# Kernel tuning notes

Measured on AMD Instinct MI355X. Metric: run time of the kernel, lower is better.

Reference implementation:

```python
import jax, jax.numpy as jnp
import numpy as np

N = 50000        # drug nodes
R = 64           # relations (side effects)
E = 20000        # edges per relation
B = 16           # bases
IN = 256
OUT = 256


def setup_inputs() -> dict:
    key = jax.random.key(0)
    ks = jax.random.split(key, 7)
    x = jax.random.normal(ks[0], (N, IN), dtype=jnp.float32)
    att = jax.random.normal(ks[1], (R, B), dtype=jnp.float32) / np.sqrt(B)
    basis = jax.random.normal(ks[2], (B, IN, OUT), dtype=jnp.float32) / np.sqrt(IN)
    root = jax.random.normal(ks[3], (IN, OUT), dtype=jnp.float32) / np.sqrt(IN)
    # per-destination-node degree normalizer (strictly positive, like edge counts)
    dest_deg = jax.random.uniform(ks[4], (N, 1), dtype=jnp.float32) * 9.0 + 1.0
    edge_src = jax.random.randint(ks[5], (R, E), 0, N, dtype=jnp.int64)
    edge_dst = jax.random.randint(ks[6], (R, E), 0, N, dtype=jnp.int64)
    return {"x": x, "att": att, "basis": basis, "root": root,
            "dest_deg": dest_deg, "edge_src": edge_src, "edge_dst": edge_dst}


def reference(x, att, basis, root, dest_deg, edge_src, edge_dst):
    # basis decomposition: w[r] = sum_b att[r,b] * basis[b]
    w = jnp.einsum('rb,bio->rio', att, basis)          # [R, IN, OUT]
    # per-relation gather + transform: messages along each edge
    x_src = x[edge_src]                                 # [R, E, IN]
    msgs = jnp.einsum('rei,rio->reo', x_src, w)         # [R, E, OUT]
    # scatter-sum to destinations, summed over all relations (HeteroConv aggr='sum')
    agg = jax.ops.segment_sum(msgs.reshape(-1, OUT),
                              edge_dst.reshape(-1),
                              num_segments=N)           # [N, OUT]
    out = agg / dest_deg + x @ root                     # [N, OUT]
    return out
```

## Files before the change

### kernel.cpp

```cpp
#include <hip/hip_runtime.h>
#include <stdint.h>

#define NN 50000
#define RR 64
#define EE 20000
#define NB 16
#define IND 256
#define OUTD 256
#define KK 4352
#define NE (RR * EE)
#define GITER 68
#define SCANB 49

typedef __attribute__((ext_vector_type(8))) short bf16x8;
typedef __attribute__((ext_vector_type(4))) float f32x4;
typedef __attribute__((ext_vector_type(2))) float f32x2;
typedef __attribute__((ext_vector_type(2))) unsigned int u32x2;

__device__ __forceinline__ unsigned short f2bf(float f) {
  union { float f; unsigned u; } v; v.f = f;
  unsigned r = v.u + 0x7FFFu + ((v.u >> 16) & 1u);
  return (unsigned short)(r >> 16);
}
__device__ __forceinline__ float asf(unsigned u) {
  union { unsigned u; float f; } v; v.u = u; return v.f;
}

__global__ __launch_bounds__(256) void k_xbf(const float* __restrict__ x,
                                             unsigned short* __restrict__ xsw) {
  const int gt = blockIdx.x * 256 + threadIdx.x;
  const size_t g = (size_t)gt * 8;
  const int row = gt >> 5;
  const int k = (gt & 31) * 8;
  float4 v0 = *reinterpret_cast<const float4*>(x + g);
  float4 v1 = *reinterpret_cast<const float4*>(x + g + 4);
  union { bf16x8 v; unsigned short u[8]; } pk;
  pk.u[0]=f2bf(v0.x); pk.u[1]=f2bf(v0.y); pk.u[2]=f2bf(v0.z); pk.u[3]=f2bf(v0.w);
  pk.u[4]=f2bf(v1.x); pk.u[5]=f2bf(v1.y); pk.u[6]=f2bf(v1.z); pk.u[7]=f2bf(v1.w);
  const int tile = k >> 6, ch = (k >> 3) & 7;
  *reinterpret_cast<bf16x8*>(
      xsw + (size_t)row * 256 + tile * 64 + ((ch ^ (row & 7)) << 3)) = pk.v;
}

__global__ __launch_bounds__(256) void k_hist(const int* __restrict__ edst,
                                              int* __restrict__ cnt) {
  const int g = blockIdx.x * 256 + threadIdx.x;
  atomicAdd(&cnt[edst[g]], 1);
}

__global__ __launch_bounds__(256) void k_scan_a(const int* __restrict__ cnt,
                                                int* __restrict__ rowptr,
                                                int* __restrict__ bsum) {
  __shared__ int ps[256];
  const int t = threadIdx.x, blk = blockIdx.x;
  const int base = blk * 1024 + t * 4;
  int v[4];
#pragma unroll
  for (int q = 0; q < 4; ++q) {
    const int idx = base + q;
    v[q] = (idx < NN) ? cnt[idx] : 0;
  }
  const int s = v[0] + v[1] + v[2] + v[3];
  ps[t] = s;
  __syncthreads();
  for (int off = 1; off < 256; off <<= 1) {
    const int u = (t >= off) ? ps[t - off] : 0;
    __syncthreads();
    ps[t] += u;
    __syncthreads();
  }
  int run = ps[t] - s;
#pragma unroll
  for (int q = 0; q < 4; ++q) {
    const int idx = base + q;
    if (idx < NN) rowptr[idx] = run;
    run += v[q];
  }
  if (t == 255) bsum[blk] = ps[255];
}

__global__ __launch_bounds__(64) void k_scan_b(const int* __restrict__ bsum,
                                               int* __restrict__ boff,
                                               int* __restrict__ rowptr) {
  const int t = threadIdx.x;
  const int own = (t < SCANB) ? bsum[t] : 0;
  int v = own;
  for (int off = 1; off < 64; off <<= 1) {
    const int u = __shfl_up(v, off);
    if (t >= off) v += u;
  }
  if (t < SCANB) boff[t] = v - own;
  if (t == SCANB - 1) rowptr[NN] = v;
}

__global__ __launch_bounds__(256) void k_scan_c(const int* __restrict__ boff,
                                                int* __restrict__ rowptr,
                                                int* __restrict__ wof) {
  const int t = threadIdx.x, blk = blockIdx.x;
  const int base = blk * 1024 + t * 4;
  const int bo = boff[blk];
#pragma unroll
  for (int q = 0; q < 4; ++q) {
    const int idx = base + q;
    if (idx < NN) {
      const int val = rowptr[idx] + bo;
      rowptr[idx] = val;
      wof[idx] = val;
    }
  }
}

__global__ __launch_bounds__(256) void k_scatter(const int* __restrict__ esrc,
                                                 const int* __restrict__ edst,
                                                 int* __restrict__ wof,
                                                 unsigned* __restrict__ payload) {
  const int g = blockIdx.x * 256 + threadIdx.x;
  const int d = edst[g];
  const int src = esrc[g];
  const int r = g / EE;
  const int pos = atomicAdd(&wof[d], 1);
  payload[pos] = ((unsigned)r << 18) | (unsigned)src;
}

__global__ __launch_bounds__(256) void k_bt(const float* __restrict__ basis,
                                            const float* __restrict__ root,
                                            unsigned short* __restrict__ bt) {
  const int o = blockIdx.x;
  for (int k = threadIdx.x; k < KK; k += 256) {
    float v;
    if (k < 4096) v = basis[(size_t)k * 256 + o];
    else          v = root[(size_t)(k - 4096) * 256 + o];
    const int tile = k >> 6, ch = (k >> 3) & 7;
    bt[(size_t)o * KK + tile * 64 + ((ch ^ (o & 7)) << 3) + (k & 7)] = f2bf(v);
  }
}

__global__ __launch_bounds__(128) void k_vbuild(
    const unsigned short* __restrict__ xsw, const float* __restrict__ att,
    const float* __restrict__ deg, const int* __restrict__ rowptr,
    const unsigned* __restrict__ payload, unsigned short* __restrict__ Vb,
    const int c0) {
  __shared__ float attl[RR * NB];
  const int t = threadIdx.x;
  *reinterpret_cast<float4*>(&attl[t * 8]) =
      *reinterpret_cast<const float4*>(&att[t * 8]);
  *reinterpret_cast<float4*>(&attl[t * 8 + 4]) =
      *reinterpret_cast<const float4*>(&att[t * 8 + 4]);
  __syncthreads();
  const int lane = t & 63;
  const int n = c0 + blockIdx.x * 2 + (t >> 6);
  if (n >= NN) return;
  const int k0 = rowptr[n], k1 = rowptr[n + 1];

  const int laneBase = (lane >> 4) * 64 + (lane & 1) * 4;
  const unsigned laneCh = (unsigned)((lane >> 1) & 7);

  f32x2 acc2[NB][2];
#pragma unroll
  for (int b = 0; b < NB; ++b) {
    acc2[b][0] = (f32x2){0.f, 0.f};
    acc2[b][1] = (f32x2){0.f, 0.f};
  }

#define XLOAD(PK)                                                            \
  (*reinterpret_cast<const uint2*>(                                          \
      xsw + (size_t)((PK) & 0x3FFFFu) * 256 + laneBase +                     \
      ((laneCh ^ ((PK) & 7u)) << 3)))

#define PROC(J, PK, XV)                                                      \
  {                                                                          \
    const bool ok_ = (k + (J)) < k1;                                         \
    const unsigned mx_ = ok_ ? (XV).x : 0u;                                  \
    const unsigned my_ = ok_ ? (XV).y : 0u;                                  \
    const int r_ = (int)((PK) >> 18);                                        \
    const f32x2 x01_ = {asf(mx_ << 16), asf(mx_ & 0xFFFF0000u)};             \
    const f32x2 x23_ = {asf(my_ << 16), asf(my_ & 0xFFFF0000u)};             \
    _Pragma("unroll")                                                        \
    for (int b4 = 0; b4 < 4; ++b4) {                                         \
      const float4 a4 = *reinterpret_cast<const float4*>(&attl[r_ * NB + b4 * 4]); \
      const float aa[4] = {a4.x, a4.y, a4.z, a4.w};                          \
      _Pragma("unroll")                                                      \
      for (int q = 0; q < 4; ++q) {                                          \
        const int b = b4 * 4 + q;                                            \
        acc2[b][0] += aa[q] * x01_;                                          \
        acc2[b][1] += aa[q] * x23_;                                          \
      }                                                                      \
    }                                                                        \
  }

  unsigned p0 = payload[k0],     p1 = payload[k0 + 1];
  unsigned p2 = payload[k0 + 2], p3 = payload[k0 + 3];
  uint2 x0 = XLOAD(p0), x1 = XLOAD(p1), x2 = XLOAD(p2), x3 = XLOAD(p3);
  unsigned q0 = payload[k0 + 4], q1 = payload[k0 + 5];
  unsigned q2 = payload[k0 + 6], q3 = payload[k0 + 7];

  for (int k = k0; k < k1; k += 4) {
    const uint2 nx0 = XLOAD(q0), nx1 = XLOAD(q1);
    const uint2 nx2 = XLOAD(q2), nx3 = XLOAD(q3);
    const unsigned r0 = payload[k + 8],  r1 = payload[k + 9];
    const unsigned r2 = payload[k + 10], r3 = payload[k + 11];
    PROC(0, p0, x0) PROC(1, p1, x1) PROC(2, p2, x2) PROC(3, p3, x3)
    p0 = q0; p1 = q1; p2 = q2; p3 = q3;
    q0 = r0; q1 = r1; q2 = r2; q3 = r3;
    x0 = nx0; x1 = nx1; x2 = nx2; x3 = nx3;
  }

  const float iv = 1.0f / deg[n];
  const int nl = n - c0;
  unsigned short* vr = Vb + (size_t)nl * 4096 + (lane >> 4) * 64 +
                       ((((unsigned)(lane >> 1) & 7u) ^ (unsigned)(nl & 7)) << 3) +
                       (lane & 1) * 4;
#pragma unroll
  for (int b = 0; b < NB; ++b) {
    const unsigned short s0 = f2bf(acc2[b][0].x * iv);
    const unsigned short s1 = f2bf(acc2[b][0].y * iv);
    const unsigned short s2 = f2bf(acc2[b][1].x * iv);
    const unsigned short s3 = f2bf(acc2[b][1].y * iv);
    u32x2 pk;
    pk.x = (unsigned)s0 | ((unsigned)s1 << 16);
    pk.y = (unsigned)s2 | ((unsigned)s3 << 16);
    __builtin_nontemporal_store(pk, reinterpret_cast<u32x2*>(vr + (size_t)b * 256));
  }
}

__global__ __launch_bounds__(256) void k_gemm4(
    const unsigned short* __restrict__ Vb, const unsigned short* __restrict__ xsw,
    const unsigned short* __restrict__ bt, float* __restrict__ out, const int c0) {
  __shared__ unsigned short As[2][128 * 64];
  __shared__ unsigned short Bs[2][128 * 64];
  const int t = threadIdx.x;
  const int rb = blockIdx.x, cb = blockIdx.y;
  const int lane = t & 63, w = t >> 6;
  const int wr = w >> 1, wc = w & 1;
  const int lc = lane & 15, lg = lane >> 4;

  const int lrow8 = lane >> 3;
  const int lchk  = lane & 7;
  const int arow0 = rb * 128 + w * 32 + lrow8;
  const int bcol0 = cb * 128 + w * 32 + lrow8;
  const unsigned short* vrow = Vb  + (size_t)arow0 * 4096 + lchk * 8;
  const unsigned short* xrow = xsw + (size_t)(c0 + arow0) * 256 + lchk * 8;
  const unsigned short* brow = bt  + (size_t)bcol0 * KK + lchk * 8;

#define GL(G, L) __builtin_amdgcn_global_load_lds(                            \
    (const __attribute__((address_space(1))) unsigned int*)(G),               \
    (__attribute__((address_space(3))) unsigned int*)(L), 16, 0, 0)

#define STAGE4(IT, BUF)                                                       \
  {                                                                           \
    const int it_ = (IT);                                                     \
    unsigned short* abase = &As[BUF][w * 2048];                               \
    unsigned short* bbase = &Bs[BUF][w * 2048];                               \
    if (it_ < 64) {                                                           \
      const unsigned short* ga = vrow + it_ * 64;                             \
      _Pragma("unroll")                                                       \
      for (int i = 0; i < 4; ++i) GL(ga + (size_t)i * 8 * 4096, abase + i * 512); \
    } else {                                                                  \
      const unsigned short* ga = xrow + (it_ - 64) * 64;                      \
      _Pragma("unroll")                                                       \
      for (int i = 0; i < 4; ++i) GL(ga + (size_t)i * 8 * 256, abase + i * 512); \
    }                                                                         \
    const unsigned short* gb = brow + it_ * 64;                               \
    _Pragma("unroll")                                                         \
    for (int i = 0; i < 4; ++i) GL(gb + (size_t)i * 8 * KK, bbase + i * 512); \
  }

  f32x4 acc[4][4];
  const f32x4 zf = {0.f, 0.f, 0.f, 0.f};
#pragma unroll
  for (int m = 0; m < 4; ++m)
#pragma unroll
    for (int n = 0; n < 4; ++n) acc[m][n] = zf;

  STAGE4(0, 0);
  asm volatile("s_waitcnt vmcnt(0)" ::: "memory");
  __syncthreads();
  int cur = 0;
  for (int it = 0; it < GITER; ++it) {
    if (it + 1 < GITER) STAGE4(it + 1, cur ^ 1);
#pragma unroll
    for (int kk = 0; kk < 2; ++kk) {
      bf16x8 af[4], bfm[4];
      const int ch = kk * 4 + lg;
#pragma unroll
      for (int m = 0; m < 4; ++m) {
        const int r2 = wr * 64 + m * 16 + lc;
        af[m] = *reinterpret_cast<const bf16x8*>(&As[cur][r2 * 64 + ((ch ^ (r2 & 7)) << 3)]);
      }
#pragma unroll
      for (int n = 0; n < 4; ++n) {
        const int c2 = wc * 64 + n * 16 + lc;
        bfm[n] = *reinterpret_cast<const bf16x8*>(&Bs[cur][c2 * 64 + ((ch ^ (c2 & 7)) << 3)]);
      }
#pragma unroll
      for (int m = 0; m < 4; ++m)
#pragma unroll
        for (int n = 0; n < 4; ++n)
          acc[m][n] = __builtin_amdgcn_mfma_f32_16x16x32_bf16(af[m], bfm[n], acc[m][n], 0, 0, 0);
    }
    asm volatile("s_waitcnt vmcnt(0)" ::: "memory");
    __syncthreads();
    cur ^= 1;
  }
#pragma unroll
  for (int m = 0; m < 4; ++m) {
#pragma unroll
    for (int j = 0; j < 4; ++j) {
      const int n = c0 + rb * 128 + wr * 64 + m * 16 + lg * 4 + j;
      if (n < NN) {
        float* orow = out + (size_t)n * OUTD + cb * 128 + wc * 64 + lc;
        __builtin_nontemporal_store(acc[m][0][j], orow + 0);
        __builtin_nontemporal_store(acc[m][1][j], orow + 16);
        __builtin_nontemporal_store(acc[m][2][j], orow + 32);
        __builtin_nontemporal_store(acc[m][3][j], orow + 48);
      }
    }
  }
}

extern "C" void kernel_launch(void* const* d_in, const int* in_sizes, int n_in,
                              void* d_out, int out_size, void* d_ws, size_t ws_size,
                              hipStream_t stream) {
  (void)in_sizes; (void)n_in; (void)out_size;
  const float* x     = (const float*)d_in[0];
  const float* att   = (const float*)d_in[1];
  const float* basis = (const float*)d_in[2];
  const float* root  = (const float*)d_in[3];
  const float* deg   = (const float*)d_in[4];
  const int*   esrc  = (const int*)d_in[5];
  const int*   edst  = (const int*)d_in[6];
  float* out = (float*)d_out;

  char* p = (char*)d_ws;
  unsigned short* xsw  = (unsigned short*)p; p += (size_t)NN * IND * 2;
  unsigned short* bt   = (unsigned short*)p; p += (size_t)OUTD * KK * 2;
  unsigned* payload    = (unsigned*)p;       p += (size_t)(NE + 16) * 4;
  int* rowptr          = (int*)p;            p += (size_t)(NN + 1) * 4;
  int* wof             = (int*)p;            p += (size_t)NN * 4;
  int* cnt             = (int*)p;            p += (size_t)NN * 4;
  int* bsum            = (int*)p;            p += 64 * 4;
  int* boff            = (int*)p;            p += 64 * 4;
  uintptr_t up = ((uintptr_t)p + 255) & ~(uintptr_t)255;
  unsigned short* Vb  = (unsigned short*)up;
  const size_t used = (size_t)((char*)Vb - (char*)d_ws);
  const size_t avail = ws_size - used;

  int chunk;
  if      (avail >= (size_t)(NN + 128) * 4096 * 2) chunk = NN;
  else if (avail >= (size_t)25600 * 4096 * 2)      chunk = 25600;
  else                                             chunk = 12800;

  hipMemsetAsync(cnt, 0, (size_t)NN * 4, stream);
  hipMemsetAsync(payload + NE, 0, 64, stream);
  hipLaunchKernelGGL(k_xbf,     dim3(NN * IND / 2048), dim3(256),  0, stream, x, xsw);
  hipLaunchKernelGGL(k_hist,    dim3(NE / 256),        dim3(256),  0, stream, edst, cnt);
  hipLaunchKernelGGL(k_scan_a,  dim3(SCANB),           dim3(256),  0, stream, cnt, rowptr, bsum);
  hipLaunchKernelGGL(k_scan_b,  dim3(1),               dim3(64),   0, stream, bsum, boff, rowptr);
  hipLaunchKernelGGL(k_scan_c,  dim3(SCANB),           dim3(256),  0, stream, boff, rowptr, wof);
  hipLaunchKernelGGL(k_scatter, dim3(NE / 256),        dim3(256),  0, stream, esrc, edst, wof, payload);
  hipLaunchKernelGGL(k_bt,      dim3(OUTD),            dim3(256),  0, stream, basis, root, bt);

  for (int c0 = 0; c0 < NN; c0 += chunk) {
    const int rows = (NN - c0 < chunk) ? (NN - c0) : chunk;
    hipLaunchKernelGGL(k_vbuild, dim3((rows + 1) / 2), dim3(128), 0, stream,
                       xsw, att, deg, rowptr, payload, Vb, c0);
    hipLaunchKernelGGL(k_gemm4, dim3((rows + 127) / 128, 2), dim3(256), 0, stream,
                       Vb, xsw, bt, out, c0);
  }
}
```

Before: 573.0 us.

## Shrink GEMM tile to 64x128 with two waves and drop LDS double buffering

Replaces the 128x128, 4-wave double-buffered GEMM with a 64x128 tile computed by 2 waves using a single LDS buffer, and synchronises before and after each stage load. Halving the tile doubles the grid and cuts LDS per block so more blocks can be resident at once. In exchange, loads no longer overlap compute within a block, and the B tile is now read from global memory twice as often because row tiles are smaller.

Result: slower. 595.9 us, median of 3 (+4.0%).

```diff
diff --git a/kernel.cpp b/kernel.cpp
--- a/kernel.cpp
+++ b/kernel.cpp
@@ -223,46 +223,52 @@
   }
 }
 
-__global__ __launch_bounds__(256) void k_gemm4(
+__global__ __launch_bounds__(128) void k_gemm6(
     const unsigned short* __restrict__ Vb, const unsigned short* __restrict__ xsw,
     const unsigned short* __restrict__ bt, float* __restrict__ out, const int c0) {
-  __shared__ unsigned short As[2][128 * 64];
-  __shared__ unsigned short Bs[2][128 * 64];
+  __shared__ unsigned short As[64 * 64];
+  __shared__ unsigned short Bs[128 * 64];
   const int t = threadIdx.x;
   const int rb = blockIdx.x, cb = blockIdx.y;
   const int lane = t & 63, w = t >> 6;
-  const int wr = w >> 1, wc = w & 1;
   const int lc = lane & 15, lg = lane >> 4;
 
-  const int lrow8 = lane >> 3;
-  const int lchk  = lane & 7;
-  const int arow0 = rb * 128 + w * 32 + lrow8;
-  const int bcol0 = cb * 128 + w * 32 + lrow8;
-  const unsigned short* vrow = Vb  + (size_t)arow0 * 4096 + lchk * 8;
-  const unsigned short* xrow = xsw + (size_t)(c0 + arow0) * 256 + lchk * 8;
-  const unsigned short* brow = bt  + (size_t)bcol0 * KK + lchk * 8;
+  const int srow = t >> 3;
+  const int spos = t & 7;
+  const unsigned short* va[4];
+  const unsigned short* xa[4];
+  const unsigned short* bb[8];
+#pragma unroll
+  for (int a = 0; a < 4; ++a) {
+    const int rl = a * 16 + srow;
+    va[a] = Vb  + (size_t)(rb * 64 + rl) * 4096 + spos * 8;
+    xa[a] = xsw + (size_t)(c0 + rb * 64 + rl) * 256 + spos * 8;
+  }
+#pragma unroll
+  for (int b = 0; b < 8; ++b) {
+    const int cl = b * 16 + srow;
+    bb[b] = bt + (size_t)(cb * 128 + cl) * KK + spos * 8;
+  }
 
 #define GL(G, L) __builtin_amdgcn_global_load_lds(                            \
     (const __attribute__((address_space(1))) unsigned int*)(G),               \
     (__attribute__((address_space(3))) unsigned int*)(L), 16, 0, 0)
 
-#define STAGE4(IT, BUF)                                                       \
+#define STAGE6(IT)                                                            \
   {                                                                           \
     const int it_ = (IT);                                                     \
-    unsigned short* abase = &As[BUF][w * 2048];                               \
-    unsigned short* bbase = &Bs[BUF][w * 2048];                               \
     if (it_ < 64) {                                                           \
-      const unsigned short* ga = vrow + it_ * 64;                             \
       _Pragma("unroll")                                                       \
-      for (int i = 0; i < 4; ++i) GL(ga + (size_t)i * 8 * 4096, abase + i * 512); \
+      for (int a = 0; a < 4; ++a)                                             \
+        GL(va[a] + it_ * 64, As + a * 1024 + (w << 9));                       \
     } else {                                                                  \
-      const unsigned short* ga = xrow + (it_ - 64) * 64;                      \
       _Pragma("unroll")                                                       \
-      for (int i = 0; i < 4; ++i) GL(ga + (size_t)i * 8 * 256, abase + i * 512); \
+      for (int a = 0; a < 4; ++a)                                             \
+        GL(xa[a] + (it_ - 64) * 64, As + a * 1024 + (w << 9));                \
     }                                                                         \
-    const unsigned short* gb = brow + it_ * 64;                               \
     _Pragma("unroll")                                                         \
-    for (int i = 0; i < 4; ++i) GL(gb + (size_t)i * 8 * KK, bbase + i * 512); \
+    for (int b = 0; b < 8; ++b)                                               \
+      GL(bb[b] + it_ * 64, Bs + b * 1024 + (w << 9));                         \
   }
 
   f32x4 acc[4][4];
@@ -272,25 +278,24 @@
 #pragma unroll
     for (int n = 0; n < 4; ++n) acc[m][n] = zf;
 
-  STAGE4(0, 0);
-  asm volatile("s_waitcnt vmcnt(0)" ::: "memory");
-  __syncthreads();
-  int cur = 0;
   for (int it = 0; it < GITER; ++it) {
-    if (it + 1 < GITER) STAGE4(it + 1, cur ^ 1);
+    __syncthreads();
+    STAGE6(it);
+    asm volatile("s_waitcnt vmcnt(0)" ::: "memory");
+    __syncthreads();
 #pragma unroll
     for (int kk = 0; kk < 2; ++kk) {
       bf16x8 af[4], bfm[4];
       const int ch = kk * 4 + lg;
 #pragma unroll
       for (int m = 0; m < 4; ++m) {
-        const int r2 = wr * 64 + m * 16 + lc;
-        af[m] = *reinterpret_cast<const bf16x8*>(&As[cur][r2 * 64 + ((ch ^ (r2 & 7)) << 3)]);
+        const int r2 = m * 16 + lc;
+        af[m] = *reinterpret_cast<const bf16x8*>(&As[r2 * 64 + ((ch ^ (r2 & 7)) << 3)]);
       }
 #pragma unroll
       for (int n = 0; n < 4; ++n) {
-        const int c2 = wc * 64 + n * 16 + lc;
-        bfm[n] = *reinterpret_cast<const bf16x8*>(&Bs[cur][c2 * 64 + ((ch ^ (c2 & 7)) << 3)]);
+        const int c2 = w * 64 + n * 16 + lc;
+        bfm[n] = *reinterpret_cast<const bf16x8*>(&Bs[c2 * 64 + ((ch ^ (c2 & 7)) << 3)]);
       }
 #pragma unroll
       for (int m = 0; m < 4; ++m)
@@ -298,17 +303,14 @@
         for (int n = 0; n < 4; ++n)
           acc[m][n] = __builtin_amdgcn_mfma_f32_16x16x32_bf16(af[m], bfm[n], acc[m][n], 0, 0, 0);
     }
-    asm volatile("s_waitcnt vmcnt(0)" ::: "memory");
-    __syncthreads();
-    cur ^= 1;
   }
 #pragma unroll
   for (int m = 0; m < 4; ++m) {
 #pragma unroll
     for (int j = 0; j < 4; ++j) {
-      const int n = c0 + rb * 128 + wr * 64 + m * 16 + lg * 4 + j;
+      const int n = c0 + rb * 64 + m * 16 + lg * 4 + j;
       if (n < NN) {
-        float* orow = out + (size_t)n * OUTD + cb * 128 + wc * 64 + lc;
+        float* orow = out + (size_t)n * OUTD + cb * 128 + w * 64 + lc;
         __builtin_nontemporal_store(acc[m][0][j], orow + 0);
         __builtin_nontemporal_store(acc[m][1][j], orow + 16);
         __builtin_nontemporal_store(acc[m][2][j], orow + 32);
@@ -364,7 +366,7 @@
     const int rows = (NN - c0 < chunk) ? (NN - c0) : chunk;
     hipLaunchKernelGGL(k_vbuild, dim3((rows + 1) / 2), dim3(128), 0, stream,
                        xsw, att, deg, rowptr, payload, Vb, c0);
-    hipLaunchKernelGGL(k_gemm4, dim3((rows + 127) / 128, 2), dim3(256), 0, stream,
+    hipLaunchKernelGGL(k_gemm6, dim3((rows + 63) / 64, 2), dim3(128), 0, stream,
                        Vb, xsw, bt, out, c0);
   }
 }
```
